# Kernel tuning notes

Measured on AMD Instinct MI355X. Metric: run time of the kernel, lower is better.

Reference implementation:

```python
import jax, jax.numpy as jnp
import numpy as np
import math

D_MODEL = 1024
N_HEADS = 16
D_HEAD = D_MODEL // N_HEADS  # 64, even (required for RoPE)
MAX_LEN = 1024


def _rope_cache(max_len, d_head, dtype=jnp.float32):
    half = d_head // 2
    inv_freq = jnp.exp(jnp.arange(half, dtype=dtype) * (-math.log(10000.0) / half))
    angles = jnp.arange(max_len, dtype=dtype)[:, None] * inv_freq[None, :]  # [max_len, half]
    return jnp.cos(angles), jnp.sin(angles)


def _apply_rope(t, cos, sin):
    # t: [B, H, L, D]; rotate-by-halves variant (cat of halves, not interleave)
    L = t.shape[2]
    half = t.shape[-1] // 2
    c = cos[:L, :half][None, None, :, :].astype(t.dtype)
    s = sin[:L, :half][None, None, :, :].astype(t.dtype)
    t1, t2 = t[..., :half], t[..., half:]
    return jnp.concatenate([t1 * c - t2 * s, t1 * s + t2 * c], axis=-1)


def setup_inputs() -> dict:
    key = jax.random.key(0)
    ks = jax.random.split(key, 11)
    B, L = 4, 1024
    std = 1.0 / math.sqrt(D_MODEL)
    return {
        "queries": jax.random.normal(ks[0], (B, L, D_MODEL), jnp.float32),
        "keys": jax.random.normal(ks[1], (B, L, D_MODEL), jnp.float32),
        "values": jax.random.normal(ks[2], (B, L, D_MODEL), jnp.float32),
        "Wq": jax.random.normal(ks[3], (D_MODEL, D_MODEL), jnp.float32) * std,
        "bq": jnp.zeros((D_MODEL,), jnp.float32),
        "Wk": jax.random.normal(ks[4], (D_MODEL, D_MODEL), jnp.float32) * std,
        "bk": jnp.zeros((D_MODEL,), jnp.float32),
        "Wv": jax.random.normal(ks[5], (D_MODEL, D_MODEL), jnp.float32) * std,
        "bv": jnp.zeros((D_MODEL,), jnp.float32),
        "Wo": jax.random.normal(ks[6], (D_MODEL, D_MODEL), jnp.float32) * std,
        "bo": jnp.zeros((D_MODEL,), jnp.float32),
    }


def reference(queries, keys, values, Wq, bq, Wk, bk, Wv, bv, Wo, bo):
    B, L, _ = queries.shape
    S = keys.shape[1]
    H, Dh = N_HEADS, D_HEAD
    cos, sin = _rope_cache(MAX_LEN, Dh, queries.dtype)

    q = (queries @ Wq + bq).reshape(B, L, H, Dh).transpose(0, 2, 1, 3)  # [B,H,L,Dh]
    k = (keys @ Wk + bk).reshape(B, S, H, Dh).transpose(0, 2, 1, 3)
    v = (values @ Wv + bv).reshape(B, S, H, Dh).transpose(0, 2, 1, 3)

    q = _apply_rope(q, cos, sin)
    k = _apply_rope(k, cos, sin)

    scores = jnp.einsum('bhid,bhjd->bhij', q, k) / math.sqrt(Dh)
    attn = jax.nn.softmax(scores, axis=-1)  # dropout is identity in eval
    out = jnp.einsum('bhij,bhjd->bhid', attn, v)  # [B,H,L,Dh]
    out = out.transpose(0, 2, 1, 3).reshape(B, L, H * Dh)
    return out @ Wo + bo
```

## Files before the change

kernel.cpp:

```cpp
#include <hip/hip_runtime.h>
#include <math.h>

#define BB 4
#define LL 1024
#define HH 16
#define DH 64
#define DM 1024
#define MM (BB * LL)

typedef short bf16x8 __attribute__((ext_vector_type(8)));
typedef float f32x4  __attribute__((ext_vector_type(4)));
typedef unsigned short u16x4 __attribute__((ext_vector_type(4)));

__device__ __forceinline__ unsigned short f2bf(float x) {
    union { float f; unsigned u; } v; v.f = x;
    unsigned r = v.u + 0x7fff + ((v.u >> 16) & 1);
    return (unsigned short)(r >> 16);
}

__device__ __forceinline__ void gl2lds16(const unsigned short* g, unsigned short* l) {
    __builtin_amdgcn_global_load_lds(
        (const __attribute__((address_space(1))) unsigned int*)g,
        (__attribute__((address_space(3))) unsigned int*)l, 16, 0, 0);
}

__global__ __launch_bounds__(256) void cvt_bf16_kernel(
    const float* __restrict__ i0, const float* __restrict__ i1, const float* __restrict__ i2,
    unsigned short* __restrict__ o0, unsigned short* __restrict__ o1, unsigned short* __restrict__ o2,
    float* __restrict__ ct, float* __restrict__ st)
{
    int z = blockIdx.z;
    if (z == 3) {
        int idx = blockIdx.x * 256 + threadIdx.x;
        if (idx < LL * 32) {
            int l = idx >> 5, d = idx & 31;
            const float coef = -0.28782313662425583f;
            float ang = (float)l * expf((float)d * coef);
            float s, c;
            sincosf(ang, &s, &c);
            ct[idx] = c;
            st[idx] = s;
        }
        return;
    }
    const float* in = (z == 0) ? i0 : (z == 1) ? i1 : i2;
    unsigned short* out = (z == 0) ? o0 : (z == 1) ? o1 : o2;
    int i = (blockIdx.x * 256 + threadIdx.x) * 4;
    float4 f = *(const float4*)(in + i);
    u16x4 r;
    r.x = f2bf(f.x); r.y = f2bf(f.y); r.z = f2bf(f.z); r.w = f2bf(f.w);
    *(u16x4*)(out + i) = r;
}

__global__ __launch_bounds__(256) void transpose_w_kernel(
    const float* __restrict__ w0, const float* __restrict__ w1,
    const float* __restrict__ w2, const float* __restrict__ w3,
    unsigned short* __restrict__ t0, unsigned short* __restrict__ t1,
    unsigned short* __restrict__ t2, unsigned short* __restrict__ t3)
{
    int z = blockIdx.z;
    const float* in = (z == 0) ? w0 : (z == 1) ? w1 : (z == 2) ? w2 : w3;
    unsigned short* out = (z == 0) ? t0 : (z == 1) ? t1 : (z == 2) ? t2 : t3;
    __shared__ float tile[32][33];
    int tx = threadIdx.x & 31, ty = threadIdx.x >> 5;
    int c0 = blockIdx.x * 32, r0 = blockIdx.y * 32;
    #pragma unroll
    for (int j = 0; j < 32; j += 8)
        tile[ty + j][tx] = in[(size_t)(r0 + ty + j) * 1024 + c0 + tx];
    __syncthreads();
    #pragma unroll
    for (int j = 0; j < 32; j += 8)
        out[(size_t)(c0 + ty + j) * 1024 + r0 + tx] = f2bf(tile[tx][ty + j]);
}

__device__ __forceinline__ void gemm128_core(
    const unsigned short* __restrict__ A, const unsigned short* __restrict__ Bt,
    unsigned short* As, unsigned short* Bs, int tM, int tN, f32x4 (&acc)[4][4])
{
    const int tid  = threadIdx.x;
    const int wave = tid >> 6, lane = tid & 63;
    const int g = lane >> 4, lm = lane & 15;
    const int wm = wave >> 1, wn = wave & 1;
    const int lr = lane >> 3, lk = lane & 7;
    const int kbl = lk ^ lr;

    for (int kt = 0; kt < 16; ++kt) {
        const int k0 = kt * 64;
        if (kt) __syncthreads();
        #pragma unroll
        for (int it = 0; it < 4; ++it) {
            int rbase = wave * 32 + it * 8;
            int r = rbase + lr;
            gl2lds16(A  + (size_t)(tM + r) * 1024 + k0 + kbl * 8, As + rbase * 64);
            gl2lds16(Bt + (size_t)(tN + r) * 1024 + k0 + kbl * 8, Bs + rbase * 64);
        }
        __syncthreads();

        #pragma unroll
        for (int kk = 0; kk < 2; ++kk) {
            bf16x8 a[4], b[4];
            const int sw = ((kk * 4 + g) ^ (lm & 7)) * 8;
            #pragma unroll
            for (int mt = 0; mt < 4; ++mt)
                a[mt] = *(const bf16x8*)&As[(wm * 64 + mt * 16 + lm) * 64 + sw];
            #pragma unroll
            for (int nt = 0; nt < 4; ++nt)
                b[nt] = *(const bf16x8*)&Bs[(wn * 64 + nt * 16 + lm) * 64 + sw];
            #pragma unroll
            for (int mt = 0; mt < 4; ++mt)
                #pragma unroll
                for (int nt = 0; nt < 4; ++nt)
                    acc[mt][nt] = __builtin_amdgcn_mfma_f32_16x16x32_bf16(
                        a[mt], b[nt], acc[mt][nt], 0, 0, 0);
        }
    }
}

__global__ __launch_bounds__(256) void gemm_qkv_kernel(
    const unsigned short* __restrict__ Aq, const unsigned short* __restrict__ Ak,
    const unsigned short* __restrict__ Av,
    const unsigned short* __restrict__ Wqt, const unsigned short* __restrict__ Wkt,
    const unsigned short* __restrict__ Wvt,
    const float* __restrict__ bq, const float* __restrict__ bk, const float* __restrict__ bv,
    const float* __restrict__ ct, const float* __restrict__ st,
    unsigned short* __restrict__ oq, unsigned short* __restrict__ ok,
    unsigned short* __restrict__ vt)
{
    __shared__ __align__(16) unsigned short As[128 * 64];
    __shared__ __align__(16) unsigned short Bs[128 * 64];

    const int z = blockIdx.z;
    const unsigned short* A  = (z == 0) ? Aq  : (z == 1) ? Ak  : Av;
    const unsigned short* Bt = (z == 0) ? Wqt : (z == 1) ? Wkt : Wvt;
    const float* bias        = (z == 0) ? bq  : (z == 1) ? bk  : bv;

    const int tM = blockIdx.y * 128, tN = blockIdx.x * 128;
    f32x4 acc[4][4] = {};
    gemm128_core(A, Bt, As, Bs, tM, tN, acc);

    const int wave = threadIdx.x >> 6, lane = threadIdx.x & 63;
    const int g = lane >> 4, lm = lane & 15;
    const int wm = wave >> 1, wn = wave & 1;

    const int colbase = tN + wn * 64;
    const int h = colbase >> 6;
    float bvv[4];
    #pragma unroll
    for (int nt = 0; nt < 4; ++nt) bvv[nt] = bias[colbase + nt * 16 + lm];

    if (z == 2) {
        #pragma unroll
        for (int mt = 0; mt < 4; ++mt) {
            int row0 = tM + wm * 64 + mt * 16 + g * 4;
            int b = row0 >> 10, l0 = row0 & 1023;
            #pragma unroll
            for (int nt = 0; nt < 4; ++nt) {
                int dloc = nt * 16 + lm;
                u16x4 p4;
                #pragma unroll
                for (int r = 0; r < 4; ++r)
                    p4[r] = f2bf(acc[mt][nt][r] + bvv[nt]);
                *(u16x4*)(vt + (((size_t)(b * HH + h) * DH + dloc) << 10) + l0) = p4;
            }
        }
    } else {
        unsigned short* out = (z == 0) ? oq : ok;
        const float sc = (z == 0) ? 0.125f * 1.4426950408889634f : 1.0f;
        #pragma unroll
        for (int mt = 0; mt < 4; ++mt)
            #pragma unroll
            for (int r = 0; r < 4; ++r) {
                int row = tM + wm * 64 + mt * 16 + g * 4 + r;
                int b = row >> 10, l = row & 1023;
                const float* cl = ct + l * 32;
                const float* sl = st + l * 32;
                unsigned short* orow = out + ((size_t)(b * HH + h) * LL + l) * DH;
                #pragma unroll
                for (int nt = 0; nt < 2; ++nt) {
                    float t1 = acc[mt][nt][r]     + bvv[nt];
                    float t2 = acc[mt][nt + 2][r] + bvv[nt + 2];
                    float c = cl[nt * 16 + lm];
                    float s = sl[nt * 16 + lm];
                    orow[nt * 16 + lm]      = f2bf((t1 * c - t2 * s) * sc);
                    orow[nt * 16 + lm + 32] = f2bf((t1 * s + t2 * c) * sc);
                }
            }
    }
}

__global__ __launch_bounds__(256) void gemm_out_kernel(
    const unsigned short* __restrict__ A, const unsigned short* __restrict__ Bt,
    const float* __restrict__ bias, float* __restrict__ C)
{
    __shared__ __align__(16) unsigned short As[128 * 64];
    __shared__ __align__(16) unsigned short Bs[128 * 64];

    const int tM = blockIdx.y * 128, tN = blockIdx.x * 128;
    f32x4 acc[4][4] = {};
    gemm128_core(A, Bt, As, Bs, tM, tN, acc);

    const int wave = threadIdx.x >> 6, lane = threadIdx.x & 63;
    const int g = lane >> 4, lm = lane & 15;
    const int wm = wave >> 1, wn = wave & 1;

    float bvv[4];
    #pragma unroll
    for (int nt = 0; nt < 4; ++nt) bvv[nt] = bias[tN + wn * 64 + nt * 16 + lm];
    #pragma unroll
    for (int mt = 0; mt < 4; ++mt)
        #pragma unroll
        for (int r = 0; r < 4; ++r) {
            int row = tM + wm * 64 + mt * 16 + g * 4 + r;
            float* crow = C + (size_t)row * DM + tN + wn * 64;
            #pragma unroll
            for (int nt = 0; nt < 4; ++nt)
                crow[nt * 16 + lm] = acc[mt][nt][r] + bvv[nt];
        }
}

#define PSTR 72

__global__ __launch_bounds__(256) void attn_mfma_kernel(
    const unsigned short* __restrict__ q, const unsigned short* __restrict__ k,
    const unsigned short* __restrict__ vt, unsigned short* __restrict__ ctx)
{
    __shared__ __align__(16) unsigned short Ks[64 * 64];
    __shared__ __align__(16) unsigned short Vs[64 * 64];
    __shared__ __align__(16) unsigned short Pb[4][16 * PSTR];

    const int tid  = threadIdx.x;
    const int wave = tid >> 6, lane = tid & 63;
    const int g = lane >> 4, lm = lane & 15;
    const int lr = lane >> 3, lk = lane & 7;
    const int kbl = lk ^ lr;
    const int n = blockIdx.x;
    const int bh = n & 63;
    const int qbase = (n >> 6) * 64;

    const unsigned short* qg  = q  + (size_t)(bh * LL + qbase) * DH;
    const unsigned short* kg  = k  + (size_t)bh * LL * DH;
    const unsigned short* vtg = vt + (size_t)bh * DH * LL;

    bf16x8 aq[2];
    {
        const unsigned short* qrow = qg + (wave * 16 + lm) * DH;
        aq[0] = *(const bf16x8*)(qrow + g * 8);
        aq[1] = *(const bf16x8*)(qrow + 32 + g * 8);
    }

    f32x4 acc[4] = {};
    float lsum = 0.f;

    for (int kt = 0; kt < 16; ++kt) {
        if (kt) __syncthreads();
        #pragma unroll
        for (int it = 0; it < 2; ++it) {
            int rbase = wave * 16 + it * 8;
            int r = rbase + lr;
            gl2lds16(kg  + (size_t)(kt * 64 + r) * DH + kbl * 8, Ks + rbase * 64);
            gl2lds16(vtg + (size_t)r * LL + kt * 64 + kbl * 8,  Vs + rbase * 64);
        }
        __syncthreads();

        f32x4 s[4] = {};
        #pragma unroll
        for (int kk = 0; kk < 2; ++kk) {
            const int sw = ((kk * 4 + g) ^ (lm & 7)) * 8;
            #pragma unroll
            for (int t = 0; t < 4; ++t) {
                bf16x8 ak = *(const bf16x8*)&Ks[(t * 16 + lm) * 64 + sw];
                s[t] = __builtin_amdgcn_mfma_f32_16x16x32_bf16(ak, aq[kk], s[t], 0, 0, 0);
            }
        }

        #pragma unroll
        for (int t = 0; t < 4; ++t) {
            u16x4 p4;
            #pragma unroll
            for (int r = 0; r < 4; ++r) {
                float p = exp2f(s[t][r]);
                lsum += p;
                p4[r] = f2bf(p);
            }
            *(u16x4*)&Pb[wave][lm * PSTR + t * 16 + g * 4] = p4;
        }

        #pragma unroll
        for (int kk = 0; kk < 2; ++kk) {
            const int sw = ((kk * 4 + g) ^ (lm & 7)) * 8;
            bf16x8 ap = *(const bf16x8*)&Pb[wave][lm * PSTR + kk * 32 + g * 8];
            #pragma unroll
            for (int dt = 0; dt < 4; ++dt) {
                bf16x8 bv = *(const bf16x8*)&Vs[(dt * 16 + lm) * 64 + sw];
                acc[dt] = __builtin_amdgcn_mfma_f32_16x16x32_bf16(ap, bv, acc[dt], 0, 0, 0);
            }
        }
    }

    float ts = lsum;
    ts += __shfl_xor(ts, 16, 64);
    ts += __shfl_xor(ts, 32, 64);

    int b = bh >> 4, h = bh & 15;
    #pragma unroll
    for (int r = 0; r < 4; ++r) {
        float inv = 1.f / __shfl(ts, g * 4 + r, 64);
        int qrow = qbase + wave * 16 + g * 4 + r;
        unsigned short* orow = ctx + (size_t)(b * LL + qrow) * DM + h * DH;
        #pragma unroll
        for (int dt = 0; dt < 4; ++dt)
            orow[dt * 16 + lm] = f2bf(acc[dt][r] * inv);
    }
}

extern "C" void kernel_launch(void* const* d_in, const int* in_sizes, int n_in,
                              void* d_out, int out_size, void* d_ws, size_t ws_size,
                              hipStream_t stream) {
    const float* queries = (const float*)d_in[0];
    const float* keys    = (const float*)d_in[1];
    const float* values  = (const float*)d_in[2];
    const float* Wq = (const float*)d_in[3];
    const float* bq = (const float*)d_in[4];
    const float* Wk = (const float*)d_in[5];
    const float* bk = (const float*)d_in[6];
    const float* Wv = (const float*)d_in[7];
    const float* bv = (const float*)d_in[8];
    const float* Wo = (const float*)d_in[9];
    const float* bo = (const float*)d_in[10];
    float* out = (float*)d_out;

    unsigned short* qb   = (unsigned short*)d_ws;
    unsigned short* kb_  = qb  + (size_t)MM * DM;
    unsigned short* vb_  = kb_ + (size_t)MM * DM;
    unsigned short* Wqt  = vb_ + (size_t)MM * DM;
    unsigned short* Wkt  = Wqt + (size_t)DM * DM;
    unsigned short* Wvt  = Wkt + (size_t)DM * DM;
    unsigned short* Wot  = Wvt + (size_t)DM * DM;
    unsigned short* q_ws = Wot + (size_t)DM * DM;
    unsigned short* k_ws = q_ws + (size_t)MM * DM;
    unsigned short* vt   = k_ws + (size_t)MM * DM;
    unsigned short* ctx  = vt   + (size_t)MM * DM;
    float* rope_cos = (float*)ctx;
    float* rope_sin = rope_cos + LL * 32;

    cvt_bf16_kernel<<<dim3(MM * DM / 1024, 1, 4), 256, 0, stream>>>(
        queries, keys, values, qb, kb_, vb_, rope_cos, rope_sin);
    transpose_w_kernel<<<dim3(32, 32, 4), 256, 0, stream>>>(
        Wq, Wk, Wv, Wo, Wqt, Wkt, Wvt, Wot);
    gemm_qkv_kernel<<<dim3(DM / 128, MM / 128, 3), 256, 0, stream>>>(
        qb, kb_, vb_, Wqt, Wkt, Wvt, bq, bk, bv, rope_cos, rope_sin,
        q_ws, k_ws, vt);
    attn_mfma_kernel<<<dim3(LL / 64 * BB * HH), 256, 0, stream>>>(
        q_ws, k_ws, vt, ctx);
    gemm_out_kernel<<<dim3(DM / 128, MM / 128), 256, 0, stream>>>(
        ctx, Wot, bo, out);
}
```

Baseline: 222.3 us.

## Double-buffer LDS tiles in GEMM and attention, add grouped tile mapping

The GEMM core and the attention kernel now use two LDS buffers per operand. Loads for the next K/V or K-slice tile are issued before the MFMAs on the current tile, and there is one barrier per iteration, so global-to-LDS copies can overlap compute. The GEMM grids become 1D with a swizzled tile mapping that groups 8 M-tiles per N column to improve L2 reuse. LDS use per block doubles, which may lower occupancy.

```diff
diff --git a/kernel.cpp b/kernel.cpp
--- a/kernel.cpp
+++ b/kernel.cpp
@@ -73,9 +73,25 @@
         out[(size_t)(c0 + ty + j) * 1024 + r0 + tx] = f2bf(tile[tx][ty + j]);
 }
 
+__device__ __forceinline__ void stage_tile(
+    const unsigned short* __restrict__ A, const unsigned short* __restrict__ Bt,
+    unsigned short* As, unsigned short* Bs, int tM, int tN, int kt,
+    int wave, int lr, int kbl)
+{
+    const int k0 = kt * 64;
+    #pragma unroll
+    for (int it = 0; it < 4; ++it) {
+        int rbase = wave * 32 + it * 8;
+        int r = rbase + lr;
+        gl2lds16(A  + (size_t)(tM + r) * 1024 + k0 + kbl * 8, As + rbase * 64);
+        gl2lds16(Bt + (size_t)(tN + r) * 1024 + k0 + kbl * 8, Bs + rbase * 64);
+    }
+}
+
 __device__ __forceinline__ void gemm128_core(
     const unsigned short* __restrict__ A, const unsigned short* __restrict__ Bt,
-    unsigned short* As, unsigned short* Bs, int tM, int tN, f32x4 (&acc)[4][4])
+    unsigned short* As, unsigned short* Bs,
+    int tM, int tN, f32x4 (&acc)[4][4])
 {
     const int tid  = threadIdx.x;
     const int wave = tid >> 6, lane = tid & 63;
@@ -84,17 +100,17 @@
     const int lr = lane >> 3, lk = lane & 7;
     const int kbl = lk ^ lr;
 
+    stage_tile(A, Bt, As, Bs, tM, tN, 0, wave, lr, kbl);
+    __syncthreads();
+
     for (int kt = 0; kt < 16; ++kt) {
-        const int k0 = kt * 64;
-        if (kt) __syncthreads();
-        #pragma unroll
-        for (int it = 0; it < 4; ++it) {
-            int rbase = wave * 32 + it * 8;
-            int r = rbase + lr;
-            gl2lds16(A  + (size_t)(tM + r) * 1024 + k0 + kbl * 8, As + rbase * 64);
-            gl2lds16(Bt + (size_t)(tN + r) * 1024 + k0 + kbl * 8, Bs + rbase * 64);
-        }
-        __syncthreads();
+        unsigned short* Ac = As + (kt & 1) * (128 * 64);
+        unsigned short* Bc = Bs + (kt & 1) * (128 * 64);
+        if (kt + 1 < 16) {
+            unsigned short* An = As + ((kt + 1) & 1) * (128 * 64);
+            unsigned short* Bn = Bs + ((kt + 1) & 1) * (128 * 64);
+            stage_tile(A, Bt, An, Bn, tM, tN, kt + 1, wave, lr, kbl);
+        }
 
         #pragma unroll
         for (int kk = 0; kk < 2; ++kk) {
@@ -102,10 +118,10 @@
             const int sw = ((kk * 4 + g) ^ (lm & 7)) * 8;
             #pragma unroll
             for (int mt = 0; mt < 4; ++mt)
-                a[mt] = *(const bf16x8*)&As[(wm * 64 + mt * 16 + lm) * 64 + sw];
+                a[mt] = *(const bf16x8*)&Ac[(wm * 64 + mt * 16 + lm) * 64 + sw];
             #pragma unroll
             for (int nt = 0; nt < 4; ++nt)
-                b[nt] = *(const bf16x8*)&Bs[(wn * 64 + nt * 16 + lm) * 64 + sw];
+                b[nt] = *(const bf16x8*)&Bc[(wn * 64 + nt * 16 + lm) * 64 + sw];
             #pragma unroll
             for (int mt = 0; mt < 4; ++mt)
                 #pragma unroll
@@ -113,7 +129,13 @@
                     acc[mt][nt] = __builtin_amdgcn_mfma_f32_16x16x32_bf16(
                         a[mt], b[nt], acc[mt][nt], 0, 0, 0);
         }
-    }
+        __syncthreads();
+    }
+}
+
+__device__ __forceinline__ void tile_map(int n, int& tM, int& tN) {
+    tM = ((n >> 6) * 8 + (n & 7)) * 128;
+    tN = ((n >> 3) & 7) * 128;
 }
 
 __global__ __launch_bounds__(256) void gemm_qkv_kernel(
@@ -126,15 +148,16 @@
     unsigned short* __restrict__ oq, unsigned short* __restrict__ ok,
     unsigned short* __restrict__ vt)
 {
-    __shared__ __align__(16) unsigned short As[128 * 64];
-    __shared__ __align__(16) unsigned short Bs[128 * 64];
+    __shared__ __align__(16) unsigned short As[2 * 128 * 64];
+    __shared__ __align__(16) unsigned short Bs[2 * 128 * 64];
 
     const int z = blockIdx.z;
     const unsigned short* A  = (z == 0) ? Aq  : (z == 1) ? Ak  : Av;
     const unsigned short* Bt = (z == 0) ? Wqt : (z == 1) ? Wkt : Wvt;
     const float* bias        = (z == 0) ? bq  : (z == 1) ? bk  : bv;
 
-    const int tM = blockIdx.y * 128, tN = blockIdx.x * 128;
+    int tM, tN;
+    tile_map(blockIdx.x, tM, tN);
     f32x4 acc[4][4] = {};
     gemm128_core(A, Bt, As, Bs, tM, tN, acc);
 
@@ -192,10 +215,11 @@
     const unsigned short* __restrict__ A, const unsigned short* __restrict__ Bt,
     const float* __restrict__ bias, float* __restrict__ C)
 {
-    __shared__ __align__(16) unsigned short As[128 * 64];
-    __shared__ __align__(16) unsigned short Bs[128 * 64];
-
-    const int tM = blockIdx.y * 128, tN = blockIdx.x * 128;
+    __shared__ __align__(16) unsigned short As[2 * 128 * 64];
+    __shared__ __align__(16) unsigned short Bs[2 * 128 * 64];
+
+    int tM, tN;
+    tile_map(blockIdx.x, tM, tN);
     f32x4 acc[4][4] = {};
     gemm128_core(A, Bt, As, Bs, tM, tN, acc);
 
@@ -224,8 +248,8 @@
     const unsigned short* __restrict__ q, const unsigned short* __restrict__ k,
     const unsigned short* __restrict__ vt, unsigned short* __restrict__ ctx)
 {
-    __shared__ __align__(16) unsigned short Ks[64 * 64];
-    __shared__ __align__(16) unsigned short Vs[64 * 64];
+    __shared__ __align__(16) unsigned short Ks[2 * 64 * 64];
+    __shared__ __align__(16) unsigned short Vs[2 * 64 * 64];
     __shared__ __align__(16) unsigned short Pb[4][16 * PSTR];
 
     const int tid  = threadIdx.x;
@@ -248,19 +272,32 @@
         aq[1] = *(const bf16x8*)(qrow + 32 + g * 8);
     }
 
+    #pragma unroll
+    for (int it = 0; it < 2; ++it) {
+        int rbase = wave * 16 + it * 8;
+        int r = rbase + lr;
+        gl2lds16(kg  + (size_t)r * DH + kbl * 8,      Ks + rbase * 64);
+        gl2lds16(vtg + (size_t)r * LL + kbl * 8,      Vs + rbase * 64);
+    }
+    __syncthreads();
+
     f32x4 acc[4] = {};
     float lsum = 0.f;
 
     for (int kt = 0; kt < 16; ++kt) {
-        if (kt) __syncthreads();
-        #pragma unroll
-        for (int it = 0; it < 2; ++it) {
-            int rbase = wave * 16 + it * 8;
-            int r = rbase + lr;
-            gl2lds16(kg  + (size_t)(kt * 64 + r) * DH + kbl * 8, Ks + rbase * 64);
-            gl2lds16(vtg + (size_t)r * LL + kt * 64 + kbl * 8,  Vs + rbase * 64);
-        }
-        __syncthreads();
+        unsigned short* Kc = Ks + (kt & 1) * (64 * 64);
+        unsigned short* Vc = Vs + (kt & 1) * (64 * 64);
+        if (kt + 1 < 16) {
+            unsigned short* Kn = Ks + ((kt + 1) & 1) * (64 * 64);
+            unsigned short* Vn = Vs + ((kt + 1) & 1) * (64 * 64);
+            #pragma unroll
+            for (int it = 0; it < 2; ++it) {
+                int rbase = wave * 16 + it * 8;
+                int r = rbase + lr;
+                gl2lds16(kg  + (size_t)((kt + 1) * 64 + r) * DH + kbl * 8, Kn + rbase * 64);
+                gl2lds16(vtg + (size_t)r * LL + (kt + 1) * 64 + kbl * 8,   Vn + rbase * 64);
+            }
+        }
 
         f32x4 s[4] = {};
         #pragma unroll
@@ -268,7 +305,7 @@
             const int sw = ((kk * 4 + g) ^ (lm & 7)) * 8;
             #pragma unroll
             for (int t = 0; t < 4; ++t) {
-                bf16x8 ak = *(const bf16x8*)&Ks[(t * 16 + lm) * 64 + sw];
+                bf16x8 ak = *(const bf16x8*)&Kc[(t * 16 + lm) * 64 + sw];
                 s[t] = __builtin_amdgcn_mfma_f32_16x16x32_bf16(ak, aq[kk], s[t], 0, 0, 0);
             }
         }
@@ -291,10 +328,11 @@
             bf16x8 ap = *(const bf16x8*)&Pb[wave][lm * PSTR + kk * 32 + g * 8];
             #pragma unroll
             for (int dt = 0; dt < 4; ++dt) {
-                bf16x8 bv = *(const bf16x8*)&Vs[(dt * 16 + lm) * 64 + sw];
+                bf16x8 bv = *(const bf16x8*)&Vc[(dt * 16 + lm) * 64 + sw];
                 acc[dt] = __builtin_amdgcn_mfma_f32_16x16x32_bf16(ap, bv, acc[dt], 0, 0, 0);
             }
         }
+        __syncthreads();
     }
 
     float ts = lsum;
@@ -347,11 +385,11 @@
         queries, keys, values, qb, kb_, vb_, rope_cos, rope_sin);
     transpose_w_kernel<<<dim3(32, 32, 4), 256, 0, stream>>>(
         Wq, Wk, Wv, Wo, Wqt, Wkt, Wvt, Wot);
-    gemm_qkv_kernel<<<dim3(DM / 128, MM / 128, 3), 256, 0, stream>>>(
+    gemm_qkv_kernel<<<dim3(256, 1, 3), 256, 0, stream>>>(
         qb, kb_, vb_, Wqt, Wkt, Wvt, bq, bk, bv, rope_cos, rope_sin,
         q_ws, k_ws, vt);
     attn_mfma_kernel<<<dim3(LL / 64 * BB * HH), 256, 0, stream>>>(
         q_ws, k_ws, vt, ctx);
-    gemm_out_kernel<<<dim3(DM / 128, MM / 128), 256, 0, stream>>>(
+    gemm_out_kernel<<<dim3(256), 256, 0, stream>>>(
         ctx, Wot, bo, out);
 }
```

Result: slower. 229.7 us (+3.3%).
